# Kernel tuning notes

Hardware: AMD Instinct MI355X
Metric: run time of the kernel (lower is better)

The kernel has to match this reference:

```python
import jax, jax.numpy as jnp
import numpy as np

B, T, C = 4, 2048, 1024
H = 16
D = C // H  # head_size = 64


def setup_inputs() -> dict:
    key = jax.random.key(0)
    ks = jax.random.split(key, 6)
    s = 0.02
    x = jax.random.normal(ks[0], (B, T, C), dtype=jnp.float32)
    # per-head projections (bias=False), stacked over heads: [H, C, D]
    Wq = jax.random.normal(ks[1], (H, C, D), dtype=jnp.float32) * s
    Wk = jax.random.normal(ks[2], (H, C, D), dtype=jnp.float32) * s
    Wv = jax.random.normal(ks[3], (H, C, D), dtype=jnp.float32) * s
    # output projection Linear(H*D, C)
    Wo = jax.random.normal(ks[4], (H * D, C), dtype=jnp.float32) * s
    bo = jax.random.normal(ks[5], (C,), dtype=jnp.float32) * s
    return {"x": x, "Wq": Wq, "Wk": Wk, "Wv": Wv, "Wo": Wo, "bo": bo}


def reference(x, Wq, Wk, Wv, Wo, bo):
    # q,k,v: [B, H, T, D]
    q = jnp.einsum('btc,hcd->bhtd', x, Wq)
    k = jnp.einsum('btc,hcd->bhtd', x, Wk)
    v = jnp.einsum('btc,hcd->bhtd', x, Wv)
    scale = 1.0 / jnp.sqrt(jnp.asarray(D, dtype=x.dtype))
    scores = jnp.einsum('bhtd,bhsd->bhts', q, k) * scale  # [B,H,T,T]
    causal = jnp.tril(jnp.ones((T, T), dtype=bool))
    scores = jnp.where(causal, scores, jnp.asarray(-jnp.inf, dtype=scores.dtype))
    wei = jax.nn.softmax(scores, axis=-1)
    out = jnp.einsum('bhts,bhsd->bhtd', wei, v)  # [B,H,T,D]
    # concat heads along last dim (head order = module list order)
    out = jnp.transpose(out, (0, 2, 1, 3)).reshape(B, T, H * D)
    return out @ Wo + bo
```

## Files before the change

kernel.cpp:

```cpp
#include <hip/hip_runtime.h>
#include <math.h>

typedef __attribute__((ext_vector_type(8))) short short8;
typedef __attribute__((ext_vector_type(4))) short short4v;
typedef __attribute__((ext_vector_type(4))) float floatx4;

#define AS1 __attribute__((address_space(1)))
#define AS3 __attribute__((address_space(3)))

__device__ inline void gload_lds16(const short* g, short* l) {
    __builtin_amdgcn_global_load_lds((const AS1 unsigned int*)g,
                                     (AS3 unsigned int*)l, 16, 0, 0);
}

__device__ inline short f2bf(float f) {
    unsigned u = __builtin_bit_cast(unsigned, f);
    u += 0x7fffu + ((u >> 16) & 1u);
    return (short)(u >> 16);
}

__global__ __launch_bounds__(256) void conv_x(
    const float* __restrict__ x, short* __restrict__ xb)
{
    int i = (blockIdx.x * 256 + threadIdx.x) * 4;
    float4 v = *(const float4*)&x[i];
    short4v o = { f2bf(v.x), f2bf(v.y), f2bf(v.z), f2bf(v.w) };
    *(short4v*)&xb[i] = o;
}

__global__ __launch_bounds__(256) void transpose_w(
    const float* __restrict__ Wq, const float* __restrict__ Wk,
    const float* __restrict__ Wv, const float* __restrict__ Wo,
    short* __restrict__ Wall, short* __restrict__ WoT)
{
    __shared__ short T[64 * 72];
    const int kt = blockIdx.x, y = blockIdx.y;
    const int tid = threadIdx.x;
    const int lr = tid >> 2, lc = (tid & 3) * 16;
    #pragma unroll 1
    for (int m = 0; m < 4; ++m) {
        const float* src;
        float s = 1.f;
        if (m < 3) {
            const float* W = (m == 0) ? Wq : (m == 1) ? Wk : Wv;
            src = W + ((size_t)y << 16) + (size_t)(kt * 64 + lr) * 64 + lc;
            if (m == 0) s = 0.125f * 1.44269504088896f;
        } else {
            src = Wo + (size_t)(kt * 64 + lr) * 1024 + y * 64 + lc;
        }
        short8 t0, t1;
        {
            float4 v0 = *(const float4*)(src + 0);
            float4 v1 = *(const float4*)(src + 4);
            float4 v2 = *(const float4*)(src + 8);
            float4 v3 = *(const float4*)(src + 12);
            t0[0]=f2bf(v0.x*s); t0[1]=f2bf(v0.y*s); t0[2]=f2bf(v0.z*s); t0[3]=f2bf(v0.w*s);
            t0[4]=f2bf(v1.x*s); t0[5]=f2bf(v1.y*s); t0[6]=f2bf(v1.z*s); t0[7]=f2bf(v1.w*s);
            t1[0]=f2bf(v2.x*s); t1[1]=f2bf(v2.y*s); t1[2]=f2bf(v2.z*s); t1[3]=f2bf(v2.w*s);
            t1[4]=f2bf(v3.x*s); t1[5]=f2bf(v3.y*s); t1[6]=f2bf(v3.z*s); t1[7]=f2bf(v3.w*s);
        }
        *(short8*)&T[lr * 72 + lc]     = t0;
        *(short8*)&T[lr * 72 + lc + 8] = t1;
        __syncthreads();
        short8 o0, o1;
        #pragma unroll
        for (int j = 0; j < 8; ++j) o0[j] = T[(lc + j) * 72 + lr];
        #pragma unroll
        for (int j = 0; j < 8; ++j) o1[j] = T[(lc + 8 + j) * 72 + lr];
        short* dst = (m < 3)
            ? Wall + (size_t)(m * 1024 + y * 64 + lr) * 1024 + kt * 64
            : WoT  + (size_t)(y * 64 + lr) * 1024 + kt * 64;
        *(short8*)&dst[lc]     = o0;
        *(short8*)&dst[lc + 8] = o1;
        __syncthreads();
    }
}

__global__ __launch_bounds__(256) void gemm_bt(
    const short* __restrict__ A, const short* __restrict__ BT,
    short* __restrict__ C, short* __restrict__ Vt, int M, int N, int K)
{
    __shared__ short As[2][128 * 64];
    __shared__ short Bs[2][128 * 64];
    const int tid  = threadIdx.x;
    const int wid  = tid >> 6, lane = tid & 63;
    const int quad = lane >> 4, l15 = lane & 15, l7 = l15 & 7;
    const int m0 = blockIdx.x * 128, n0 = blockIdx.y * 128;
    const int wr = (wid >> 1) * 64, wc = (wid & 1) * 64;

    floatx4 acc[4][4] = {};

    const int srow = tid >> 3;
    const int gcol = ((tid & 7) ^ (srow & 7)) * 8;
    const int lrow = wid * 8;
    const int NT = K >> 6;

    const short* aCur = A  + (size_t)(m0 + srow) * K + gcol;
    const short* bCur = BT + (size_t)(n0 + srow) * K + gcol;

#define STAGE(c) do { \
    _Pragma("unroll") \
    for (int tt = 0; tt < 4; ++tt) { \
        gload_lds16(aCur + (size_t)(tt * 32) * K, &As[c][(tt * 32 + lrow) * 64]); \
        gload_lds16(bCur + (size_t)(tt * 32) * K, &Bs[c][(tt * 32 + lrow) * 64]); \
    } \
    aCur += 64; bCur += 64; } while (0)

    STAGE(0);
    __syncthreads();

    for (int t = 0; t < NT; ++t) {
        if (t + 1 < NT) STAGE((t + 1) & 1);
        const short* Ab = As[t & 1];
        const short* Bb = Bs[t & 1];
        #pragma unroll
        for (int ks = 0; ks < 2; ++ks) {
            short8 bfr[4], afr[4];
            #pragma unroll
            for (int j = 0; j < 4; ++j)
                bfr[j] = *(const short8*)&Bb[(wc + j * 16 + l15) * 64 +
                                             (((ks * 4 + quad) ^ l7) * 8)];
            #pragma unroll
            for (int i = 0; i < 4; ++i)
                afr[i] = *(const short8*)&Ab[(wr + i * 16 + l15) * 64 +
                                             (((ks * 4 + quad) ^ l7) * 8)];
            #pragma unroll
            for (int i = 0; i < 4; ++i)
                #pragma unroll
                for (int j = 0; j < 4; ++j)
                    acc[i][j] = __builtin_amdgcn_mfma_f32_16x16x32_bf16(
                        afr[i], bfr[j], acc[i][j], 0, 0, 0);
        }
        __syncthreads();
    }
#undef STAGE

    const int plane = n0 >> 10;
    #pragma unroll
    for (int i = 0; i < 4; ++i) {
        int row = m0 + wr + i * 16 + quad * 4;
        #pragma unroll
        for (int j = 0; j < 4; ++j) {
            int col = n0 + wc + j * 16 + l15;
            int c1 = col & 1023;
            if (plane < 2) {
                short* dst = C + (size_t)plane * 8192 * 1024;
                #pragma unroll
                for (int r = 0; r < 4; ++r)
                    dst[(size_t)(row + r) * 1024 + c1] = f2bf(acc[i][j][r]);
            } else {
                int b = row >> 11, t = row & 2047;
                int hb = b * 16 + (c1 >> 6), d = c1 & 63;
                short4v o = { f2bf(acc[i][j][0]), f2bf(acc[i][j][1]),
                              f2bf(acc[i][j][2]), f2bf(acc[i][j][3]) };
                *(short4v*)&Vt[((size_t)hb * 64 + d) * 2048 + t] = o;
            }
        }
    }
}

__global__ __launch_bounds__(256) void gemm_o(
    const short* __restrict__ A, const short* __restrict__ BT,
    float* __restrict__ Cf, const float* __restrict__ bias, int N, int K)
{
    __shared__ short As[64 * 64];
    __shared__ short Bs[128 * 64];
    const int tid  = threadIdx.x;
    const int wid  = tid >> 6, lane = tid & 63;
    const int quad = lane >> 4, l15 = lane & 15;
    const int l7 = l15 & 7;
    const int m0 = blockIdx.x * 64, n0 = blockIdx.y * 128;
    const int wr = (wid >> 1) * 32, wc = (wid & 1) * 64;

    floatx4 acc[2][4] = {};

    const int srow = tid >> 3;
    const int gcol = ((tid & 7) ^ (srow & 7)) * 8;

    for (int k0 = 0; k0 < K; k0 += 64) {
        #pragma unroll
        for (int t = 0; t < 2; ++t)
            gload_lds16(A + (size_t)(m0 + srow + t * 32) * K + k0 + gcol,
                        &As[(t * 32 + wid * 8) * 64]);
        #pragma unroll
        for (int t = 0; t < 4; ++t)
            gload_lds16(BT + (size_t)(n0 + srow + t * 32) * K + k0 + gcol,
                        &Bs[(t * 32 + wid * 8) * 64]);
        __syncthreads();
        #pragma unroll
        for (int ks = 0; ks < 2; ++ks) {
            short8 bfr[4];
            #pragma unroll
            for (int j = 0; j < 4; ++j)
                bfr[j] = *(const short8*)&Bs[(wc + j * 16 + l15) * 64 +
                                             (((ks * 4 + quad) ^ l7) * 8)];
            #pragma unroll
            for (int i = 0; i < 2; ++i) {
                short8 afr = *(const short8*)&As[(wr + i * 16 + l15) * 64 +
                                                 (((ks * 4 + quad) ^ l7) * 8)];
                #pragma unroll
                for (int j = 0; j < 4; ++j)
                    acc[i][j] = __builtin_amdgcn_mfma_f32_16x16x32_bf16(
                        afr, bfr[j], acc[i][j], 0, 0, 0);
            }
        }
        __syncthreads();
    }

    #pragma unroll
    for (int i = 0; i < 2; ++i) {
        int row = m0 + wr + i * 16 + quad * 4;
        #pragma unroll
        for (int j = 0; j < 4; ++j) {
            int col = n0 + wc + j * 16 + l15;
            float bv = bias[col];
            #pragma unroll
            for (int r = 0; r < 4; ++r)
                Cf[(size_t)(row + r) * N + col] = acc[i][j][r] + bv;
        }
    }
}

__global__ __launch_bounds__(256) void attn_fwd(
    const short* __restrict__ Q, const short* __restrict__ Kg,
    const short* __restrict__ Vt_g, short* __restrict__ O)
{
    __shared__ short Ks[2][64 * 64];
    __shared__ short Vs[2][64 * 64];
    __shared__ short Pb[4 * 32 * 72];
    const int tid  = threadIdx.x;
    const int wid  = tid >> 6, lane = tid & 63;
    const int quad = lane >> 4, l15 = lane & 15;

    const int flat = blockIdx.x;
    const int xr = flat & 7;
    const int qq = flat >> 3;
    const int qt = 15 - (qq >> 3);
    const int hb = xr * 8 + (qq & 7);
    const int h = hb & 15, b = hb >> 4;

    const size_t base  = ((size_t)b * 2048) * 1024 + h * 64;
    const size_t vbase = ((size_t)(b * 16 + h)) * 64 * 2048;
    short* Pw = &Pb[wid * 32 * 72];

    const int srow = tid >> 3;
    const int gcol = ((tid & 7) ^ (srow & 7)) * 8;
    const int lbase0 = (wid * 8) * 64;
    const int lbase1 = (wid * 8 + 32) * 64;
    const int l7 = l15 & 7;

    const short one_bf = (short)0x3F80;
    const short8 bones = { one_bf, one_bf, one_bf, one_bf,
                           one_bf, one_bf, one_bf, one_bf };

    short8 qf[2][2];
    #pragma unroll
    for (int mt = 0; mt < 2; ++mt)
        #pragma unroll
        for (int ks = 0; ks < 2; ++ks)
            qf[mt][ks] = *(const short8*)&Q[base +
                (size_t)(qt * 128 + wid * 32 + mt * 16 + l15) * 1024 + ks * 32 + quad * 8];

    floatx4 oacc[2][4] = {};
    floatx4 lacc[2] = {};
    const int dst = 2 * qt + (wid >> 1);
    const int nst = 2 * qt + 2;

    const short* kptr = Kg + base + (size_t)srow * 1024 + gcol;
    const short* vptr = Vt_g + vbase + (size_t)srow * 2048 + gcol;

    gload_lds16(kptr,               &Ks[0][lbase0]);
    gload_lds16(kptr + 32 * 1024,   &Ks[0][lbase1]);
    gload_lds16(vptr,               &Vs[0][lbase0]);
    gload_lds16(vptr + 32 * 2048,   &Vs[0][lbase1]);
    kptr += 64 * 1024; vptr += 64;
    __syncthreads();

    for (int st = 0; st < nst; ++st) {
        const short* K0 = Ks[st & 1];
        const short* V0 = Vs[st & 1];
        if (st + 1 < nst) {
            short* K1 = Ks[(st + 1) & 1];
            short* V1 = Vs[(st + 1) & 1];
            gload_lds16(kptr,             &K1[lbase0]);
            gload_lds16(kptr + 32 * 1024, &K1[lbase1]);
            gload_lds16(vptr,             &V1[lbase0]);
            gload_lds16(vptr + 32 * 2048, &V1[lbase1]);
            kptr += 64 * 1024; vptr += 64;
        }

        if (st <= dst) {
            floatx4 sf[2][4];
            #pragma unroll
            for (int nt = 0; nt < 4; ++nt) {
                floatx4 z0 = {}, z1 = {};
                #pragma unroll
                for (int ks = 0; ks < 2; ++ks) {
                    short8 bfr = *(const short8*)&K0[(nt * 16 + l15) * 64 +
                                                     (((ks * 4 + quad) ^ l7) * 8)];
                    z0 = __builtin_amdgcn_mfma_f32_16x16x32_bf16(qf[0][ks], bfr, z0, 0, 0, 0);
                    z1 = __builtin_amdgcn_mfma_f32_16x16x32_bf16(qf[1][ks], bfr, z1, 0, 0, 0);
                }
                sf[0][nt] = z0; sf[1][nt] = z1;
            }

            if (st == dst) {
                #pragma unroll
                for (int mt = 0; mt < 2; ++mt)
                    #pragma unroll
                    for (int nt = 0; nt < 4; ++nt)
                        #pragma unroll
                        for (int r = 0; r < 4; ++r) {
                            int qa = qt * 128 + wid * 32 + mt * 16 + quad * 4 + r;
                            int sa = st * 64 + nt * 16 + l15;
                            if (sa > qa) sf[mt][nt][r] = -INFINITY;
                        }
            }

            #pragma unroll
            for (int mt = 0; mt < 2; ++mt)
                #pragma unroll
                for (int nt = 0; nt < 4; ++nt)
                    #pragma unroll
                    for (int r = 0; r < 4; ++r) {
                        float p = __builtin_amdgcn_exp2f(sf[mt][nt][r]);
                        unsigned u = __builtin_bit_cast(unsigned, p);
                        Pw[(mt * 16 + quad * 4 + r) * 72 + ((nt ^ quad) * 16) + l15] =
                            (short)(u >> 16);
                    }

            #pragma unroll
            for (int ks = 0; ks < 2; ++ks) {
                int blk = (ks * 2 + (quad >> 1)) ^ (l15 >> 2);
                short8 af0 = *(const short8*)&Pw[(l15) * 72 + blk * 16 + (quad & 1) * 8];
                short8 af1 = *(const short8*)&Pw[(16 + l15) * 72 + blk * 16 + (quad & 1) * 8];
                lacc[0] = __builtin_amdgcn_mfma_f32_16x16x32_bf16(af0, bones, lacc[0], 0, 0, 0);
                lacc[1] = __builtin_amdgcn_mfma_f32_16x16x32_bf16(af1, bones, lacc[1], 0, 0, 0);
                #pragma unroll
                for (int nt = 0; nt < 4; ++nt) {
                    short8 bfr = *(const short8*)&V0[(nt * 16 + l15) * 64 +
                                                     (((ks * 4 + quad) ^ l7) * 8)];
                    oacc[0][nt] = __builtin_amdgcn_mfma_f32_16x16x32_bf16(af0, bfr, oacc[0][nt], 0, 0, 0);
                    oacc[1][nt] = __builtin_amdgcn_mfma_f32_16x16x32_bf16(af1, bfr, oacc[1][nt], 0, 0, 0);
                }
            }
        }
        __syncthreads();
    }

    #pragma unroll
    for (int mt = 0; mt < 2; ++mt)
        #pragma unroll
        for (int nt = 0; nt < 4; ++nt)
            #pragma unroll
            for (int r = 0; r < 4; ++r) {
                float v = oacc[mt][nt][r] / lacc[mt][r];
                int qa = qt * 128 + wid * 32 + mt * 16 + quad * 4 + r;
                O[base + (size_t)qa * 1024 + nt * 16 + l15] = f2bf(v);
            }
}

extern "C" void kernel_launch(void* const* d_in, const int* in_sizes, int n_in,
                              void* d_out, int out_size, void* d_ws, size_t ws_size,
                              hipStream_t stream) {
    const float* x  = (const float*)d_in[0];
    const float* Wq = (const float*)d_in[1];
    const float* Wk = (const float*)d_in[2];
    const float* Wv = (const float*)d_in[3];
    const float* Wo = (const float*)d_in[4];
    const float* bo = (const float*)d_in[5];
    float* out = (float*)d_out;

    char* ws = (char*)d_ws;
    const size_t MB = 1024 * 1024;
    short* xb   = (short*)(ws + 0 * MB);
    short* Ao   = (short*)(ws + 0 * MB);
    short* Vt_g = (short*)(ws + 16 * MB);
    short* Wall = (short*)(ws + 32 * MB);
    short* WoT  = (short*)(ws + 38 * MB);
    short* Qp   = (short*)d_out;
    short* Kp   = Qp + 8 * 1024 * 1024;

    conv_x<<<8192, 256, 0, stream>>>(x, xb);
    transpose_w<<<dim3(16, 16), 256, 0, stream>>>(Wq, Wk, Wv, Wo, Wall, WoT);

    gemm_bt<<<dim3(64, 24), 256, 0, stream>>>(xb, Wall, Qp, Vt_g, 8192, 3072, 1024);

    attn_fwd<<<1024, 256, 0, stream>>>(Qp, Kp, Vt_g, Ao);

    gemm_o<<<dim3(128, 8), 256, 0, stream>>>(Ao, WoT, out, bo, 1024, 1024);
}
```

Measured before the change: 246.4 us.

## Triple-buffer QKV GEMM with vmcnt waits, XCD-aware tile mapping, MFMA priority

The QKV projection GEMM moves from double to triple buffering in LDS. Two tiles stay in flight, and explicit vmcnt waits plus raw barriers replace the per-step __syncthreads. The 2D grid becomes a 1D grid whose block index is remapped so each XCD gets a fixed set of N panels, which should improve L2 reuse of the weight tiles. s_setprio is raised around the MFMA block. The costs are 96KB of LDS, which limits the kernel to one block per CU, and manual wait counts that depend on the exact number of loads issued per stage.

```diff
diff --git a/kernel.cpp b/kernel.cpp
--- a/kernel.cpp
+++ b/kernel.cpp
@@ -76,16 +76,21 @@
     }
 }
 
-__global__ __launch_bounds__(256) void gemm_bt(
+__global__ __launch_bounds__(256, 1) void gemm_bt(
     const short* __restrict__ A, const short* __restrict__ BT,
     short* __restrict__ C, short* __restrict__ Vt, int M, int N, int K)
 {
-    __shared__ short As[2][128 * 64];
-    __shared__ short Bs[2][128 * 64];
+    __shared__ short As[3][128 * 64];
+    __shared__ short Bs[3][128 * 64];
     const int tid  = threadIdx.x;
     const int wid  = tid >> 6, lane = tid & 63;
     const int quad = lane >> 4, l15 = lane & 15, l7 = l15 & 7;
-    const int m0 = blockIdx.x * 128, n0 = blockIdx.y * 128;
+
+    const int flat = blockIdx.x;
+    const int xcd = flat & 7, local = flat >> 3;
+    const int n_panel = xcd * 3 + (local % 3);
+    const int m_panel = local / 3;
+    const int m0 = m_panel * 128, n0 = n_panel * 128;
     const int wr = (wid >> 1) * 64, wc = (wid & 1) * 64;
 
     floatx4 acc[4][4] = {};
@@ -98,7 +103,7 @@
     const short* aCur = A  + (size_t)(m0 + srow) * K + gcol;
     const short* bCur = BT + (size_t)(n0 + srow) * K + gcol;
 
-#define STAGE(c) do { \
+#define G_ISSUE(c) do { \
     _Pragma("unroll") \
     for (int tt = 0; tt < 4; ++tt) { \
         gload_lds16(aCur + (size_t)(tt * 32) * K, &As[c][(tt * 32 + lrow) * 64]); \
@@ -106,13 +111,15 @@
     } \
     aCur += 64; bCur += 64; } while (0)
 
-    STAGE(0);
-    __syncthreads();
-
+    G_ISSUE(0); G_ISSUE(1); G_ISSUE(2);
+    asm volatile("s_waitcnt vmcnt(16)" ::: "memory");
+    __builtin_amdgcn_s_barrier();
+    asm volatile("" ::: "memory");
+
+    int c = 0;
     for (int t = 0; t < NT; ++t) {
-        if (t + 1 < NT) STAGE((t + 1) & 1);
-        const short* Ab = As[t & 1];
-        const short* Bb = Bs[t & 1];
+        const short* Ab = As[c];
+        const short* Bb = Bs[c];
         #pragma unroll
         for (int ks = 0; ks < 2; ++ks) {
             short8 bfr[4], afr[4];
@@ -124,16 +131,27 @@
             for (int i = 0; i < 4; ++i)
                 afr[i] = *(const short8*)&Ab[(wr + i * 16 + l15) * 64 +
                                              (((ks * 4 + quad) ^ l7) * 8)];
+            __builtin_amdgcn_s_setprio(1);
             #pragma unroll
             for (int i = 0; i < 4; ++i)
                 #pragma unroll
                 for (int j = 0; j < 4; ++j)
                     acc[i][j] = __builtin_amdgcn_mfma_f32_16x16x32_bf16(
                         afr[i], bfr[j], acc[i][j], 0, 0, 0);
-        }
-        __syncthreads();
-    }
-#undef STAGE
+            __builtin_amdgcn_s_setprio(0);
+        }
+        asm volatile("" ::: "memory");
+        __builtin_amdgcn_s_barrier();
+        asm volatile("" ::: "memory");
+        if (t + 3 <= NT) { asm volatile("s_waitcnt vmcnt(8)" ::: "memory"); }
+        else             { asm volatile("s_waitcnt vmcnt(0)" ::: "memory"); }
+        if (t + 3 < NT) G_ISSUE(c);
+        asm volatile("" ::: "memory");
+        __builtin_amdgcn_s_barrier();
+        asm volatile("" ::: "memory");
+        c = (c == 2) ? 0 : c + 1;
+    }
+#undef G_ISSUE
 
     const int plane = n0 >> 10;
     #pragma unroll
@@ -384,7 +402,7 @@
     conv_x<<<8192, 256, 0, stream>>>(x, xb);
     transpose_w<<<dim3(16, 16), 256, 0, stream>>>(Wq, Wk, Wv, Wo, Wall, WoT);
 
-    gemm_bt<<<dim3(64, 24), 256, 0, stream>>>(xb, Wall, Qp, Vt_g, 8192, 3072, 1024);
+    gemm_bt<<<1536, 256, 0, stream>>>(xb, Wall, Qp, Vt_g, 8192, 3072, 1024);
 
     attn_fwd<<<1024, 256, 0, stream>>>(Qp, Kp, Vt_g, Ao);
 
```

Result: slower. 303.4 us (+23.2%).
